# Optimization experiments

Hardware: AMD Instinct MI355X
Metric: run time of the kernel (lower is better)

The kernel has to match this reference:

```python
import jax, jax.numpy as jnp
import numpy as np

NEG_SLOPE = 0.01
LN_EPS = 1e-5

def _layer_norm(h, g, b):
    mu = jnp.mean(h, axis=-1, keepdims=True)
    var = jnp.mean(jnp.square(h - mu), axis=-1, keepdims=True)
    return (h - mu) * jax.lax.rsqrt(var + LN_EPS) * g + b

def _mlp(h, Wa, ba, g, be, Wb, bb):
    h = h @ Wa + ba
    h = jnp.where(h >= 0, h, NEG_SLOPE * h)  # LeakyReLU
    h = _layer_norm(h, g, be)
    return h @ Wb + bb

def setup_inputs() -> dict:
    N, E = 50000, 800000
    DN, DE, DG, DO = 128, 64, 32, 128
    key = jax.random.key(0)
    ks = jax.random.split(key, 16)
    def lin(k, fan_in, fan_out):
        lim = 1.0 / np.sqrt(fan_in)
        k1, k2 = jax.random.split(k)
        W = jax.random.uniform(k1, (fan_in, fan_out), jnp.float32, -lim, lim)
        b = jax.random.uniform(k2, (fan_out,), jnp.float32, -lim, lim)
        return W, b
    W1a, b1a = lin(ks[0], DN + DE + DG, DO)
    W1b, b1b = lin(ks[1], DO, DO)
    W2a, b2a = lin(ks[2], DN + DO, DO)
    W2b, b2b = lin(ks[3], DO, DO)
    return {
        "x": jax.random.normal(ks[4], (N, DN), jnp.float32),
        "edge_index": jax.random.randint(ks[5], (2, E), 0, N, jnp.int32),
        "edge_attr": jax.random.normal(ks[6], (E, DE), jnp.float32),
        "u": jax.random.normal(ks[7], (DG,), jnp.float32),
        "batch": jnp.zeros((N,), jnp.int32),
        "W1a": W1a, "b1a": b1a,
        "g1": jnp.ones((DO,), jnp.float32), "be1": jnp.zeros((DO,), jnp.float32),
        "W1b": W1b, "b1b": b1b,
        "W2a": W2a, "b2a": b2a,
        "g2": jnp.ones((DO,), jnp.float32), "be2": jnp.zeros((DO,), jnp.float32),
        "W2b": W2b, "b2b": b2b,
    }

def reference(x, edge_index, edge_attr, u, batch,
              W1a, b1a, g1, be1, W1b, b1b,
              W2a, b2a, g2, be2, W2b, b2b):
    src, dest = edge_index[0], edge_index[1]
    E = edge_attr.shape[0]
    N = x.shape[0]
    # gather + concat: [E, DN+DE+DG]
    h = jnp.concatenate([x[src], edge_attr,
                         jnp.broadcast_to(u[None, :], (E, u.shape[0]))], axis=1)
    h = _mlp(h, W1a, b1a, g1, be1, W1b, b1b)
    # scatter_mean by dest
    sums = jax.ops.segment_sum(h, dest, num_segments=N)
    cnt = jax.ops.segment_sum(jnp.ones((E,), h.dtype), dest, num_segments=N)
    agg = sums / jnp.maximum(cnt, 1.0)[:, None]
    return _mlp(jnp.concatenate([x, agg], axis=1), W2a, b2a, g2, be2, W2b, b2b)
```

## Files before the change

### kernel.cpp

```cpp
#include <hip/hip_runtime.h>
#include <hip/hip_fp16.h>
#include <hip/hip_bf16.h>

constexpr int DN = 128, DE = 64, DG = 32, DO = 128;
constexpr int K1 = DN + DE + DG;
constexpr float NEG_SLOPE = 0.01f;
constexpr float LN_EPS = 1e-5f;

constexpr int EPB = 128;
constexpr int NB  = 64;
constexpr int T_LD = 136;
constexpr int H_LD = 132;

typedef __attribute__((ext_vector_type(8))) short bf16x8;
typedef __attribute__((ext_vector_type(4))) float f32x4;

__device__ inline unsigned short f2bf(float f) {
    unsigned u = __builtin_bit_cast(unsigned, f);
    u += 0x7FFFu + ((u >> 16) & 1u);
    return (unsigned short)(u >> 16);
}

__device__ inline bf16x8 pk8(float4 p, float4 q) {
    bf16x8 r;
    r[0] = (short)f2bf(p.x); r[1] = (short)f2bf(p.y);
    r[2] = (short)f2bf(p.z); r[3] = (short)f2bf(p.w);
    r[4] = (short)f2bf(q.x); r[5] = (short)f2bf(q.y);
    r[6] = (short)f2bf(q.z); r[7] = (short)f2bf(q.w);
    return r;
}

__global__ void wprep_kernel(const float* __restrict__ W1a,
                             const float* __restrict__ W1b,
                             const float* __restrict__ W2a,
                             const float* __restrict__ W2b,
                             const float* __restrict__ b1b,
                             unsigned short* __restrict__ tab,
                             float* __restrict__ bc) {
    int idx = blockIdx.x * 256 + threadIdx.x;
    if (idx >= 19 * 512 + 128) return;
    if (idx >= 19 * 512) {
        int n = idx - 19 * 512;
        float s = 0.f;
        for (int j = 0; j < DO; ++j) s += b1b[j] * W2a[(long)(DN + j) * DO + n];
        bc[n] = s;
        return;
    }
    int slabset = idx >> 9;
    int rem = idx & 511;
    int nt = rem >> 6, lane = rem & 63;
    int quad = lane >> 4, l15 = lane & 15;
    int n = nt * 16 + l15;
    union { ushort4 u4[2]; unsigned short s[8]; } o;
    if (slabset < 7) {
        int k0 = slabset * 32 + quad * 8;
#pragma unroll
        for (int j = 0; j < 8; ++j) o.s[j] = f2bf(W1a[(long)(k0 + j) * DO + n]);
    } else if (slabset < 11) {
        int k0 = (slabset - 7) * 32 + quad * 8;
#pragma unroll
        for (int j = 0; j < 8; ++j) o.s[j] = f2bf(W2a[(long)(k0 + j) * DO + n]);
    } else if (slabset < 15) {
        int k0 = (slabset - 11) * 32 + quad * 8;
        float s[8] = {0.f, 0.f, 0.f, 0.f, 0.f, 0.f, 0.f, 0.f};
        for (int j2 = 0; j2 < DO; ++j2) {
            float wa = W2a[(long)(DN + j2) * DO + n];
#pragma unroll
            for (int j = 0; j < 8; ++j) s[j] += W1b[(long)(k0 + j) * DO + j2] * wa;
        }
#pragma unroll
        for (int j = 0; j < 8; ++j) o.s[j] = f2bf(s[j]);
    } else {
        int k0 = (slabset - 15) * 32 + quad * 8;
#pragma unroll
        for (int j = 0; j < 8; ++j) o.s[j] = f2bf(W2b[(long)(k0 + j) * DO + n]);
    }
    *(ushort4*)&tab[(long)idx * 8]     = o.u4[0];
    *(ushort4*)&tab[(long)idx * 8 + 4] = o.u4[1];
}

__global__ void hist_kernel(const int* __restrict__ edge_index,
                            int* __restrict__ counts, int E) {
    int e = blockIdx.x * 256 + threadIdx.x;
    if (e < E) atomicAdd(&counts[edge_index[E + e]], 1);
}

__global__ __launch_bounds__(1024) void scan_kernel(
    const int* __restrict__ counts, int* __restrict__ offsets,
    int* __restrict__ cursor, int N) {
    __shared__ int s_ws[16];
    __shared__ int s_carry;
    const int tid = threadIdx.x, lane = tid & 63, wv = tid >> 6;
    if (tid == 0) s_carry = 0;
    __syncthreads();
    for (int base = 0; base < N; base += 1024) {
        int i = base + tid;
        int v = (i < N) ? counts[i] : 0;
        int s = v;
#pragma unroll
        for (int off = 1; off < 64; off <<= 1) {
            int t = __shfl_up(s, off, 64);
            if (lane >= off) s += t;
        }
        if (lane == 63) s_ws[wv] = s;
        __syncthreads();
        if (tid < 16) {
            int w = s_ws[tid];
#pragma unroll
            for (int off = 1; off < 16; off <<= 1) {
                int t = __shfl_up(w, off, 16);
                if (tid >= off) w += t;
            }
            s_ws[tid] = w;
        }
        __syncthreads();
        int carry = s_carry;
        int woff = (wv == 0) ? 0 : s_ws[wv - 1];
        int excl = carry + woff + (s - v);
        if (i < N) { offsets[i] = excl; cursor[i] = excl; }
        int total = s_ws[15];
        __syncthreads();
        if (tid == 0) s_carry = carry + total;
        __syncthreads();
    }
    if (threadIdx.x == 0) offsets[N] = s_carry;
}

__global__ void scatter_kernel(const int* __restrict__ edge_index,
                               int* __restrict__ cursor,
                               int2* __restrict__ sorted, int E) {
    int e = blockIdx.x * 256 + threadIdx.x;
    if (e < E) {
        int d = edge_index[E + e];
        int pos = atomicAdd(&cursor[d], 1);
        sorted[pos] = make_int2(e, d);
    }
}

__global__ __launch_bounds__(256) void edge_kernel(
    const float* __restrict__ x, const int* __restrict__ edge_index,
    const float* __restrict__ edge_attr, const float* __restrict__ u,
    const int2* __restrict__ sorted, const unsigned short* __restrict__ tab,
    const float* __restrict__ b1a, const float* __restrict__ g1,
    const float* __restrict__ be1,
    float* __restrict__ sums, int E)
{
    __shared__ int s_src[EPB], s_eid[EPB], s_dst[EPB];
    __shared__ alignas(16) __half s_h[EPB * H_LD];

    const int tid = threadIdx.x, lane = tid & 63, wave = tid >> 6;
    const int l15 = lane & 15, quad = lane >> 4;
    const int ebase = blockIdx.x * EPB;
    const int evalid = min(EPB, E - ebase);

    if (tid < EPB) {
        bool v = tid < evalid;
        int2 ed = v ? sorted[ebase + tid] : make_int2(0, 0);
        s_eid[tid] = ed.x;
        s_dst[tid] = ed.y;
        s_src[tid] = edge_index[ed.x];
    }
    __syncthreads();

    const int r0 = wave * 32 + l15, r1 = r0 + 16;
    const long xs0 = (long)s_src[r0] * DN;
    const long xs1 = (long)s_src[r1] * DN;
    const long er0 = (long)s_eid[r0] * DE;
    const long er1 = (long)s_eid[r1] * DE;
    const bf16x8* tW1a = (const bf16x8*)tab;
    const int kq = quad * 8;

    f32x4 acc[2][8];
#pragma unroll
    for (int mt = 0; mt < 2; ++mt)
#pragma unroll
        for (int nt = 0; nt < 8; ++nt) acc[mt][nt] = (f32x4){0.f, 0.f, 0.f, 0.f};

#pragma unroll
    for (int ks = 0; ks < 7; ++ks) {
        float4 p0, q0, p1, q1;
        if (ks < 4) {
            const float* b0 = &x[xs0 + ks * 32 + kq];
            const float* b1 = &x[xs1 + ks * 32 + kq];
            p0 = *(const float4*)b0; q0 = *(const float4*)(b0 + 4);
            p1 = *(const float4*)b1; q1 = *(const float4*)(b1 + 4);
        } else if (ks < 6) {
            int c = ks * 32 - DN + kq;
            const float* b0 = &edge_attr[er0 + c];
            const float* b1 = &edge_attr[er1 + c];
            p0 = *(const float4*)b0; q0 = *(const float4*)(b0 + 4);
            p1 = *(const float4*)b1; q1 = *(const float4*)(b1 + 4);
        } else {
            p0 = *(const float4*)&u[kq]; q0 = *(const float4*)&u[kq + 4];
            p1 = p0; q1 = q0;
        }
        bf16x8 a0 = pk8(p0, q0);
        bf16x8 a1 = pk8(p1, q1);
#pragma unroll
        for (int nt = 0; nt < 8; ++nt) {
            bf16x8 b = tW1a[(ks * 8 + nt) * 64 + lane];
            acc[0][nt] = __builtin_amdgcn_mfma_f32_16x16x32_bf16(a0, b, acc[0][nt], 0, 0, 0);
            acc[1][nt] = __builtin_amdgcn_mfma_f32_16x16x32_bf16(a1, b, acc[1][nt], 0, 0, 0);
        }
    }

    float ba[8], gg[8], bb[8];
#pragma unroll
    for (int nt = 0; nt < 8; ++nt) {
        int col = nt * 16 + l15;
        ba[nt] = b1a[col]; gg[nt] = g1[col]; bb[nt] = be1[col];
    }
#pragma unroll
    for (int mt = 0; mt < 2; ++mt) {
#pragma unroll
        for (int r = 0; r < 4; ++r) {
            float v[8];
            float s = 0.f, q = 0.f;
#pragma unroll
            for (int nt = 0; nt < 8; ++nt) {
                float t = acc[mt][nt][r] + ba[nt];
                t = (t >= 0.f) ? t : NEG_SLOPE * t;
                v[nt] = t; s += t; q += t * t;
            }
#pragma unroll
            for (int off = 1; off < 16; off <<= 1) {
                s += __shfl_xor(s, off, 64);
                q += __shfl_xor(q, off, 64);
            }
            float mu  = s * (1.f / DO);
            float var = q * (1.f / DO) - mu * mu;
            float rs  = rsqrtf(var + LN_EPS);
            int lrow = wave * 32 + mt * 16 + quad * 4 + r;
#pragma unroll
            for (int nt = 0; nt < 8; ++nt) {
                float h  = (v[nt] - mu) * rs * gg[nt] + bb[nt];
                float hp = __shfl_xor(h, 1, 64);
                if ((l15 & 1) == 0) {
                    *(__half2*)&s_h[lrow * H_LD + nt * 16 + l15] =
                        __halves2half2(__float2half_rn(h), __float2half_rn(hp));
                }
            }
        }
    }
    __syncthreads();

    {
        const int d = tid & 127, g = tid >> 7;
        int e0 = g * 64, e1 = min(e0 + 64, evalid);
        if (e0 < e1) {
            float accv = 0.f;
            int cur = s_dst[e0];
            for (int e = e0; e < e1; ++e) {
                int dd = s_dst[e];
                if (dd != cur) {
                    atomicAdd(&sums[(long)cur * DO + d], accv);
                    accv = 0.f; cur = dd;
                }
                accv += __half2float(s_h[e * H_LD + d]);
            }
            atomicAdd(&sums[(long)cur * DO + d], accv);
        }
    }
}

__global__ __launch_bounds__(256) void node_kernel(
    const float* __restrict__ x, const float* __restrict__ sums,
    const int* __restrict__ offsets, const unsigned short* __restrict__ tab,
    const float* __restrict__ bc,
    const float* __restrict__ b2a, const float* __restrict__ g2,
    const float* __restrict__ be2, const float* __restrict__ b2b,
    float* __restrict__ out, int N)
{
    __shared__ unsigned short s_t[4][16 * T_LD];

    const int tid = threadIdx.x, lane = tid & 63, wave = tid >> 6;
    const int l15 = lane & 15, quad = lane >> 4;
    const int nbase = blockIdx.x * NB;

    const bf16x8* tW2aT = (const bf16x8*)tab + 7 * 512;
    const bf16x8* tWc   = (const bf16x8*)tab + 11 * 512;
    const bf16x8* tW2b  = (const bf16x8*)tab + 15 * 512;

    const int nodeA = min(nbase + wave * 16 + l15, N - 1);
    const int cntA  = offsets[nodeA + 1] - offsets[nodeA];
    const float invc = 1.f / fmaxf((float)cntA, 1.f);
    const int kq = quad * 8;

    f32x4 acc[8];

#pragma unroll
    for (int nt = 0; nt < 8; ++nt) acc[nt] = (f32x4){0.f, 0.f, 0.f, 0.f};
#pragma unroll
    for (int ks = 0; ks < 8; ++ks) {
        bf16x8 a;
        if (ks < 4) {
            const float* b0 = &x[(long)nodeA * DN + ks * 32 + kq];
            a = pk8(*(const float4*)b0, *(const float4*)(b0 + 4));
        } else {
            const float* sp = &sums[(long)nodeA * DO + (ks - 4) * 32 + kq];
            float4 p = *(const float4*)sp;
            float4 q = *(const float4*)(sp + 4);
            p.x *= invc; p.y *= invc; p.z *= invc; p.w *= invc;
            q.x *= invc; q.y *= invc; q.z *= invc; q.w *= invc;
            a = pk8(p, q);
        }
        const bf16x8* tB = (ks < 4) ? tW2aT : tWc;
        const int kk = (ks < 4) ? ks : ks - 4;
#pragma unroll
        for (int nt = 0; nt < 8; ++nt) {
            bf16x8 b = tB[(kk * 8 + nt) * 64 + lane];
            acc[nt] = __builtin_amdgcn_mfma_f32_16x16x32_bf16(a, b, acc[nt], 0, 0, 0);
        }
    }
    {
        float ba[8], gg[8], bb[8], bcv[8];
#pragma unroll
        for (int nt = 0; nt < 8; ++nt) {
            int col = nt * 16 + l15;
            ba[nt] = b2a[col]; gg[nt] = g2[col]; bb[nt] = be2[col]; bcv[nt] = bc[col];
        }
#pragma unroll
        for (int reg = 0; reg < 4; ++reg) {
            int nodeC = nbase + wave * 16 + quad * 4 + reg;
            int cc = (nodeC < N) ? (offsets[nodeC + 1] - offsets[nodeC]) : 0;
            float cf = (cc > 0) ? 1.f : 0.f;
            float v[8];
            float s = 0.f, q = 0.f;
#pragma unroll
            for (int nt = 0; nt < 8; ++nt) {
                float t = acc[nt][reg] + ba[nt] + cf * bcv[nt];
                t = (t >= 0.f) ? t : NEG_SLOPE * t;
                v[nt] = t; s += t; q += t * t;
            }
#pragma unroll
            for (int off = 1; off < 16; off <<= 1) {
                s += __shfl_xor(s, off, 64);
                q += __shfl_xor(q, off, 64);
            }
            float mu  = s * (1.f / DO);
            float var = q * (1.f / DO) - mu * mu;
            float rs  = rsqrtf(var + LN_EPS);
            int lrow = quad * 4 + reg;
#pragma unroll
            for (int nt = 0; nt < 8; ++nt) {
                float h = (v[nt] - mu) * rs * gg[nt] + bb[nt];
                s_t[wave][lrow * T_LD + nt * 16 + l15] = f2bf(h);
            }
        }
    }

#pragma unroll
    for (int nt = 0; nt < 8; ++nt) acc[nt] = (f32x4){0.f, 0.f, 0.f, 0.f};
#pragma unroll
    for (int ks = 0; ks < 4; ++ks) {
        bf16x8 a = *(const bf16x8*)&s_t[wave][l15 * T_LD + ks * 32 + kq];
#pragma unroll
        for (int nt = 0; nt < 8; ++nt) {
            bf16x8 b = tW2b[(ks * 8 + nt) * 64 + lane];
            acc[nt] = __builtin_amdgcn_mfma_f32_16x16x32_bf16(a, b, acc[nt], 0, 0, 0);
        }
    }
    {
#pragma unroll
        for (int reg = 0; reg < 4; ++reg) {
            int nodeC = nbase + wave * 16 + quad * 4 + reg;
            if (nodeC < N) {
                long base = (long)nodeC * DO;
#pragma unroll
                for (int nt = 0; nt < 8; ++nt)
                    out[base + nt * 16 + l15] = acc[nt][reg] + b2b[nt * 16 + l15];
            }
        }
    }
}

extern "C" void kernel_launch(void* const* d_in, const int* in_sizes, int n_in,
                              void* d_out, int out_size, void* d_ws, size_t ws_size,
                              hipStream_t stream)
{
    const float* x          = (const float*)d_in[0];
    const int*   edge_index = (const int*)d_in[1];
    const float* edge_attr  = (const float*)d_in[2];
    const float* u          = (const float*)d_in[3];
    const float* W1a = (const float*)d_in[5];
    const float* b1a = (const float*)d_in[6];
    const float* g1  = (const float*)d_in[7];
    const float* be1 = (const float*)d_in[8];
    const float* W1b = (const float*)d_in[9];
    const float* b1b = (const float*)d_in[10];
    const float* W2a = (const float*)d_in[11];
    const float* b2a = (const float*)d_in[12];
    const float* g2  = (const float*)d_in[13];
    const float* be2 = (const float*)d_in[14];
    const float* W2b = (const float*)d_in[15];
    const float* b2b = (const float*)d_in[16];

    const int N = in_sizes[0] / DN;
    const int E = in_sizes[2] / DE;
    float* out  = (float*)d_out;

    char* p = (char*)d_ws;
    int2* sorted = (int2*)p;                      p += (size_t)E * sizeof(int2);
    unsigned short* tab = (unsigned short*)p;     p += (size_t)19 * 512 * 8 * sizeof(unsigned short);
    float* bc = (float*)p;                        p += 128 * sizeof(float);
    int* counts = (int*)p;                        p += (size_t)N * sizeof(int);
    int* offsets = (int*)p;                       p += (size_t)(N + 1) * sizeof(int);
    p = (char*)(((uintptr_t)p + 15) & ~(uintptr_t)15);
    int* cursor = (int*)p;                        p += (size_t)N * sizeof(int);
    float* sums = (float*)d_out;

    (void)hipMemsetAsync(counts, 0, (size_t)N * sizeof(int), stream);
    (void)hipMemsetAsync(d_out, 0, (size_t)N * DO * sizeof(float), stream);

    wprep_kernel<<<(19 * 512 + 128 + 255) / 256, 256, 0, stream>>>(
        W1a, W1b, W2a, W2b, b1b, tab, bc);

    hist_kernel<<<(E + 255) / 256, 256, 0, stream>>>(edge_index, counts, E);
    scan_kernel<<<1, 1024, 0, stream>>>(counts, offsets, cursor, N);
    scatter_kernel<<<(E + 255) / 256, 256, 0, stream>>>(edge_index, cursor, sorted, E);

    const int eblocks = (E + EPB - 1) / EPB;
    edge_kernel<<<eblocks, 256, 0, stream>>>(
        x, edge_index, edge_attr, u, sorted, tab, b1a, g1, be1, sums, E);

    const int nblocks = (N + NB - 1) / NB;
    node_kernel<<<nblocks, 256, 0, stream>>>(
        x, sums, offsets, tab, bc, b2a, g2, be2, b2b, out, N);
}
```

Measured before the change: 806.2 us.

## Fold global-feature term into bias, parallelize scan, vectorize segmented scatter atomics

Because u is broadcast to every edge, its contribution u·W1a[192:224] is precomputed once into a modified bias, removing one of seven MFMA k-steps from the edge GEMM. The single-block serial prefix scan over node counts is replaced with a three-kernel multi-block scan. The segmented reduce-and-atomic stage now has each wave process 32 edges with two columns per lane using half2 loads and unsafeAtomicAdd. The trade-off is two extra small kernel launches, and a possibly different float rounding in the atomics.

```diff
diff --git a/kernel.cpp b/kernel.cpp
--- a/kernel.cpp
+++ b/kernel.cpp
@@ -3,7 +3,6 @@
 #include <hip/hip_bf16.h>
 
 constexpr int DN = 128, DE = 64, DG = 32, DO = 128;
-constexpr int K1 = DN + DE + DG;
 constexpr float NEG_SLOPE = 0.01f;
 constexpr float LN_EPS = 1e-5f;
 
@@ -34,13 +33,23 @@
                              const float* __restrict__ W1b,
                              const float* __restrict__ W2a,
                              const float* __restrict__ W2b,
+                             const float* __restrict__ b1a,
                              const float* __restrict__ b1b,
+                             const float* __restrict__ u,
                              unsigned short* __restrict__ tab,
-                             float* __restrict__ bc) {
+                             float* __restrict__ bc,
+                             float* __restrict__ b1ap) {
     int idx = blockIdx.x * 256 + threadIdx.x;
-    if (idx >= 19 * 512 + 128) return;
-    if (idx >= 19 * 512) {
-        int n = idx - 19 * 512;
+    if (idx >= 18 * 512 + 256) return;
+    if (idx >= 18 * 512 + 128) {
+        int n = idx - (18 * 512 + 128);
+        float s = b1a[n];
+        for (int k = 0; k < DG; ++k) s += u[k] * W1a[(long)(192 + k) * DO + n];
+        b1ap[n] = s;
+        return;
+    }
+    if (idx >= 18 * 512) {
+        int n = idx - 18 * 512;
         float s = 0.f;
         for (int j = 0; j < DO; ++j) s += b1b[j] * W2a[(long)(DN + j) * DO + n];
         bc[n] = s;
@@ -52,16 +61,16 @@
     int quad = lane >> 4, l15 = lane & 15;
     int n = nt * 16 + l15;
     union { ushort4 u4[2]; unsigned short s[8]; } o;
-    if (slabset < 7) {
+    if (slabset < 6) {
         int k0 = slabset * 32 + quad * 8;
 #pragma unroll
         for (int j = 0; j < 8; ++j) o.s[j] = f2bf(W1a[(long)(k0 + j) * DO + n]);
-    } else if (slabset < 11) {
-        int k0 = (slabset - 7) * 32 + quad * 8;
+    } else if (slabset < 10) {
+        int k0 = (slabset - 6) * 32 + quad * 8;
 #pragma unroll
         for (int j = 0; j < 8; ++j) o.s[j] = f2bf(W2a[(long)(k0 + j) * DO + n]);
-    } else if (slabset < 15) {
-        int k0 = (slabset - 11) * 32 + quad * 8;
+    } else if (slabset < 14) {
+        int k0 = (slabset - 10) * 32 + quad * 8;
         float s[8] = {0.f, 0.f, 0.f, 0.f, 0.f, 0.f, 0.f, 0.f};
         for (int j2 = 0; j2 < DO; ++j2) {
             float wa = W2a[(long)(DN + j2) * DO + n];
@@ -71,7 +80,7 @@
 #pragma unroll
         for (int j = 0; j < 8; ++j) o.s[j] = f2bf(s[j]);
     } else {
-        int k0 = (slabset - 15) * 32 + quad * 8;
+        int k0 = (slabset - 14) * 32 + quad * 8;
 #pragma unroll
         for (int j = 0; j < 8; ++j) o.s[j] = f2bf(W2b[(long)(k0 + j) * DO + n]);
     }
@@ -85,45 +94,62 @@
     if (e < E) atomicAdd(&counts[edge_index[E + e]], 1);
 }
 
-__global__ __launch_bounds__(1024) void scan_kernel(
+__global__ __launch_bounds__(1024) void scan1_kernel(
     const int* __restrict__ counts, int* __restrict__ offsets,
-    int* __restrict__ cursor, int N) {
+    int* __restrict__ partials, int N) {
     __shared__ int s_ws[16];
-    __shared__ int s_carry;
     const int tid = threadIdx.x, lane = tid & 63, wv = tid >> 6;
-    if (tid == 0) s_carry = 0;
+    int i = blockIdx.x * 1024 + tid;
+    int v = (i < N) ? counts[i] : 0;
+    int s = v;
+#pragma unroll
+    for (int off = 1; off < 64; off <<= 1) {
+        int t = __shfl_up(s, off, 64);
+        if (lane >= off) s += t;
+    }
+    if (lane == 63) s_ws[wv] = s;
     __syncthreads();
-    for (int base = 0; base < N; base += 1024) {
-        int i = base + tid;
-        int v = (i < N) ? counts[i] : 0;
+    if (tid < 16) {
+        int w = s_ws[tid];
+#pragma unroll
+        for (int off = 1; off < 16; off <<= 1) {
+            int t = __shfl_up(w, off, 16);
+            if (tid >= off) w += t;
+        }
+        s_ws[tid] = w;
+    }
+    __syncthreads();
+    int wbase = wv ? s_ws[wv - 1] : 0;
+    if (i < N) offsets[i] = wbase + s - v;
+    if (tid == 0) partials[blockIdx.x] = s_ws[15];
+}
+
+__global__ void scan2_kernel(int* __restrict__ partials, int P) {
+    const int t = threadIdx.x;
+    int carry = 0;
+    for (int base = 0; base < P; base += 64) {
+        int idx = base + t;
+        int v = (idx < P) ? partials[idx] : 0;
         int s = v;
 #pragma unroll
         for (int off = 1; off < 64; off <<= 1) {
-            int t = __shfl_up(s, off, 64);
-            if (lane >= off) s += t;
-        }
-        if (lane == 63) s_ws[wv] = s;
-        __syncthreads();
-        if (tid < 16) {
-            int w = s_ws[tid];
-#pragma unroll
-            for (int off = 1; off < 16; off <<= 1) {
-                int t = __shfl_up(w, off, 16);
-                if (tid >= off) w += t;
-            }
-            s_ws[tid] = w;
-        }
-        __syncthreads();
-        int carry = s_carry;
-        int woff = (wv == 0) ? 0 : s_ws[wv - 1];
-        int excl = carry + woff + (s - v);
-        if (i < N) { offsets[i] = excl; cursor[i] = excl; }
-        int total = s_ws[15];
-        __syncthreads();
-        if (tid == 0) s_carry = carry + total;
-        __syncthreads();
-    }
-    if (threadIdx.x == 0) offsets[N] = s_carry;
+            int w = __shfl_up(s, off, 64);
+            if (t >= off) s += w;
+        }
+        if (idx < P) partials[idx] = carry + s - v;
+        carry += __shfl(s, 63, 64);
+    }
+}
+
+__global__ __launch_bounds__(1024) void scan3_kernel(
+    int* __restrict__ offsets, const int* __restrict__ partials,
+    int* __restrict__ cursor, int N, int E) {
+    int i = blockIdx.x * 1024 + threadIdx.x;
+    if (i < N) {
+        int o = offsets[i] + partials[blockIdx.x];
+        offsets[i] = o; cursor[i] = o;
+    }
+    if (i == 0) offsets[N] = E;
 }
 
 __global__ void scatter_kernel(const int* __restrict__ edge_index,
@@ -139,9 +165,9 @@
 
 __global__ __launch_bounds__(256) void edge_kernel(
     const float* __restrict__ x, const int* __restrict__ edge_index,
-    const float* __restrict__ edge_attr, const float* __restrict__ u,
+    const float* __restrict__ edge_attr,
     const int2* __restrict__ sorted, const unsigned short* __restrict__ tab,
-    const float* __restrict__ b1a, const float* __restrict__ g1,
+    const float* __restrict__ b1ap, const float* __restrict__ g1,
     const float* __restrict__ be1,
     float* __restrict__ sums, int E)
 {
@@ -177,22 +203,19 @@
         for (int nt = 0; nt < 8; ++nt) acc[mt][nt] = (f32x4){0.f, 0.f, 0.f, 0.f};
 
 #pragma unroll
-    for (int ks = 0; ks < 7; ++ks) {
+    for (int ks = 0; ks < 6; ++ks) {
         float4 p0, q0, p1, q1;
         if (ks < 4) {
             const float* b0 = &x[xs0 + ks * 32 + kq];
             const float* b1 = &x[xs1 + ks * 32 + kq];
             p0 = *(const float4*)b0; q0 = *(const float4*)(b0 + 4);
             p1 = *(const float4*)b1; q1 = *(const float4*)(b1 + 4);
-        } else if (ks < 6) {
+        } else {
             int c = ks * 32 - DN + kq;
             const float* b0 = &edge_attr[er0 + c];
             const float* b1 = &edge_attr[er1 + c];
             p0 = *(const float4*)b0; q0 = *(const float4*)(b0 + 4);
             p1 = *(const float4*)b1; q1 = *(const float4*)(b1 + 4);
-        } else {
-            p0 = *(const float4*)&u[kq]; q0 = *(const float4*)&u[kq + 4];
-            p1 = p0; q1 = q0;
         }
         bf16x8 a0 = pk8(p0, q0);
         bf16x8 a1 = pk8(p1, q1);
@@ -208,7 +231,7 @@
 #pragma unroll
     for (int nt = 0; nt < 8; ++nt) {
         int col = nt * 16 + l15;
-        ba[nt] = b1a[col]; gg[nt] = g1[col]; bb[nt] = be1[col];
+        ba[nt] = b1ap[col]; gg[nt] = g1[col]; bb[nt] = be1[col];
     }
 #pragma unroll
     for (int mt = 0; mt < 2; ++mt) {
@@ -245,20 +268,38 @@
     __syncthreads();
 
     {
-        const int d = tid & 127, g = tid >> 7;
-        int e0 = g * 64, e1 = min(e0 + 64, evalid);
+        const int d2 = lane * 2;
+        int e0 = wave * 32, e1 = min(e0 + 32, evalid);
         if (e0 < e1) {
-            float accv = 0.f;
+            float a0 = 0.f, a1 = 0.f;
             int cur = s_dst[e0];
-            for (int e = e0; e < e1; ++e) {
-                int dd = s_dst[e];
-                if (dd != cur) {
-                    atomicAdd(&sums[(long)cur * DO + d], accv);
-                    accv = 0.f; cur = dd;
+            if (e1 - e0 == 32) {
+#pragma unroll
+                for (int k = 0; k < 32; ++k) {
+                    int e = e0 + k;
+                    int dd = s_dst[e];
+                    if (dd != cur) {
+                        unsafeAtomicAdd(&sums[(long)cur * DO + d2], a0);
+                        unsafeAtomicAdd(&sums[(long)cur * DO + d2 + 1], a1);
+                        a0 = a1 = 0.f; cur = dd;
+                    }
+                    float2 hv = __half22float2(*(const __half2*)&s_h[e * H_LD + d2]);
+                    a0 += hv.x; a1 += hv.y;
                 }
-                accv += __half2float(s_h[e * H_LD + d]);
-            }
-            atomicAdd(&sums[(long)cur * DO + d], accv);
+            } else {
+                for (int e = e0; e < e1; ++e) {
+                    int dd = s_dst[e];
+                    if (dd != cur) {
+                        unsafeAtomicAdd(&sums[(long)cur * DO + d2], a0);
+                        unsafeAtomicAdd(&sums[(long)cur * DO + d2 + 1], a1);
+                        a0 = a1 = 0.f; cur = dd;
+                    }
+                    float2 hv = __half22float2(*(const __half2*)&s_h[e * H_LD + d2]);
+                    a0 += hv.x; a1 += hv.y;
+                }
+            }
+            unsafeAtomicAdd(&sums[(long)cur * DO + d2], a0);
+            unsafeAtomicAdd(&sums[(long)cur * DO + d2 + 1], a1);
         }
     }
 }
@@ -277,9 +318,9 @@
     const int l15 = lane & 15, quad = lane >> 4;
     const int nbase = blockIdx.x * NB;
 
-    const bf16x8* tW2aT = (const bf16x8*)tab + 7 * 512;
-    const bf16x8* tWc   = (const bf16x8*)tab + 11 * 512;
-    const bf16x8* tW2b  = (const bf16x8*)tab + 15 * 512;
+    const bf16x8* tW2aT = (const bf16x8*)tab + 6 * 512;
+    const bf16x8* tWc   = (const bf16x8*)tab + 10 * 512;
+    const bf16x8* tW2b  = (const bf16x8*)tab + 14 * 512;
 
     const int nodeA = min(nbase + wave * 16 + l15, N - 1);
     const int cntA  = offsets[nodeA + 1] - offsets[nodeA];
@@ -400,28 +441,33 @@
     float* out  = (float*)d_out;
 
     char* p = (char*)d_ws;
-    int2* sorted = (int2*)p;                      p += (size_t)E * sizeof(int2);
-    unsigned short* tab = (unsigned short*)p;     p += (size_t)19 * 512 * 8 * sizeof(unsigned short);
-    float* bc = (float*)p;                        p += 128 * sizeof(float);
-    int* counts = (int*)p;                        p += (size_t)N * sizeof(int);
-    int* offsets = (int*)p;                       p += (size_t)(N + 1) * sizeof(int);
+    int2* sorted = (int2*)p;                   p += (size_t)E * sizeof(int2);
+    unsigned short* tab = (unsigned short*)p;  p += (size_t)18 * 512 * 8 * sizeof(unsigned short);
+    float* bc = (float*)p;                     p += 128 * sizeof(float);
+    float* b1ap = (float*)p;                   p += 128 * sizeof(float);
+    int* counts = (int*)p;                     p += (size_t)N * sizeof(int);
+    int* offsets = (int*)p;                    p += (size_t)(N + 1) * sizeof(int);
     p = (char*)(((uintptr_t)p + 15) & ~(uintptr_t)15);
-    int* cursor = (int*)p;                        p += (size_t)N * sizeof(int);
+    int* partials = (int*)p;                   p += 64 * sizeof(int);
+    int* cursor = (int*)p;                     p += (size_t)N * sizeof(int);
     float* sums = (float*)d_out;
 
     (void)hipMemsetAsync(counts, 0, (size_t)N * sizeof(int), stream);
     (void)hipMemsetAsync(d_out, 0, (size_t)N * DO * sizeof(float), stream);
 
-    wprep_kernel<<<(19 * 512 + 128 + 255) / 256, 256, 0, stream>>>(
-        W1a, W1b, W2a, W2b, b1b, tab, bc);
-
+    wprep_kernel<<<(18 * 512 + 256 + 255) / 256, 256, 0, stream>>>(
+        W1a, W1b, W2a, W2b, b1a, b1b, u, tab, bc, b1ap);
+
+    const int P = (N + 1023) / 1024;
     hist_kernel<<<(E + 255) / 256, 256, 0, stream>>>(edge_index, counts, E);
-    scan_kernel<<<1, 1024, 0, stream>>>(counts, offsets, cursor, N);
+    scan1_kernel<<<P, 1024, 0, stream>>>(counts, offsets, partials, N);
+    scan2_kernel<<<1, 64, 0, stream>>>(partials, P);
+    scan3_kernel<<<P, 1024, 0, stream>>>(offsets, partials, cursor, N, E);
     scatter_kernel<<<(E + 255) / 256, 256, 0, stream>>>(edge_index, cursor, sorted, E);
 
     const int eblocks = (E + EPB - 1) / EPB;
     edge_kernel<<<eblocks, 256, 0, stream>>>(
-        x, edge_index, edge_attr, u, sorted, tab, b1a, g1, be1, sums, E);
+        x, edge_index, edge_attr, sorted, tab, b1ap, g1, be1, sums, E);
 
     const int nblocks = (N + NB - 1) / NB;
     node_kernel<<<nblocks, 256, 0, stream>>>(
```

New measurement: 728.7 us. 9.6% less time.
